# Performance work log

Hardware: AMD Instinct MI355X
Metric: run time of the kernel (lower is better)

## Reference

```python
import jax, jax.numpy as jnp
import numpy as np


def _conv(x, k):
    # x: (B,H,W,Cin), k: (kh,kw,Cin,Cout), SAME padding, stride 1
    return jax.lax.conv_general_dilated(
        x, k, window_strides=(1, 1), padding='SAME',
        dimension_numbers=('NHWC', 'HWIO', 'NHWC'))


def _hard_sigmoid(x):
    # Keras ConvLSTM2D default recurrent_activation='hard_sigmoid'
    return jnp.clip(0.2 * x + 0.5, 0.0, 1.0)


def _convlstm_layer(x_seq, k, rk, b):
    # x_seq: (B,T,H,W,Cin); gates packed i,f,c,o along channel axis (Keras order)
    B, T, H, W, _ = x_seq.shape
    F = rk.shape[2]
    h0 = jnp.zeros((B, H, W, F), x_seq.dtype)
    c0 = jnp.zeros((B, H, W, F), x_seq.dtype)

    def step(carry, xt):
        h, c = carry
        z = _conv(xt, k) + _conv(h, rk) + b
        i, f, g, o = jnp.split(z, 4, axis=-1)
        c_new = _hard_sigmoid(f) * c + _hard_sigmoid(i) * jnp.tanh(g)
        h_new = _hard_sigmoid(o) * jnp.tanh(c_new)
        return (h_new, c_new), h_new

    (h, c), ys = jax.lax.scan(step, (h0, c0), jnp.moveaxis(x_seq, 1, 0))
    return jnp.moveaxis(ys, 0, 1), h, c  # outputs (B,T,H,W,F), final h, c


def setup_inputs() -> dict:
    key = jax.random.key(0)
    ks = jax.random.split(key, 6)
    s = 0.05
    return {
        'x': jax.random.normal(ks[0], (8, 10, 64, 64, 1), jnp.float32),
        'k0': jax.random.normal(ks[1], (3, 3, 1, 256), jnp.float32) * s,
        'rk0': jax.random.normal(ks[2], (3, 3, 64, 256), jnp.float32) * s,
        'b0': jnp.zeros((256,), jnp.float32),
        'k1': jax.random.normal(ks[3], (3, 3, 64, 256), jnp.float32) * s,
        'rk1': jax.random.normal(ks[4], (3, 3, 64, 256), jnp.float32) * s,
        'b1': jnp.zeros((256,), jnp.float32),
    }


def reference(x, k0, rk0, b0, k1, rk1, b1):
    # layer 0
    seq0, h0, c0 = _convlstm_layer(x, k0, rk0, b0)
    # layer 1 consumes layer-0 sequence
    _, h1, c1 = _convlstm_layer(seq0, k1, rk1, b1)
    # states list [[h0,c0],[h1,c1]] -> stacked (layers=2, 2, B, H, W, F)
    return jnp.stack([jnp.stack([h0, c0]), jnp.stack([h1, c1])])
```

## Files before the change

### kernel.cpp

```cpp
#include <hip/hip_runtime.h>
#include <hip/hip_bf16.h>

typedef unsigned short u16;
typedef __attribute__((ext_vector_type(8))) short short8;
typedef __attribute__((ext_vector_type(4))) float f32x4;

#define T_STEPS 10
#define NB 8
#define HH 64
#define WW 64
#define FF 64
#define NGATE 256
#define HP 66
#define PIX (NB*HH*WW)
#define ROWCH 528

__device__ __forceinline__ u16 f2bf(float f) {
    unsigned u = __float_as_uint(f);
    u += 0x7FFF + ((u >> 16) & 1);
    return (u16)(u >> 16);
}
__device__ __forceinline__ float hsig(float x) {
    return fminf(fmaxf(0.2f * x + 0.5f, 0.0f), 1.0f);
}
__device__ __forceinline__ float ftanh(float x) {
    float e = __expf(2.0f * x);
    return 1.0f - 2.0f / (e + 1.0f);
}
__device__ __forceinline__ void gll16(const void* g, void* l) {
    __builtin_amdgcn_global_load_lds(
        (const __attribute__((address_space(1))) unsigned*)g,
        (__attribute__((address_space(3))) unsigned*)l, 16, 0, 0);
}

__global__ void wtrans_kernel(const float* __restrict__ W0,
                              const float* __restrict__ W1,
                              u16* __restrict__ BS, int K) {
    int total = (K >> 6) << 14;
    for (int o = blockIdx.x * blockDim.x + threadIdx.x; o < total;
         o += gridDim.x * blockDim.x) {
        int e = o & 7, lane = (o >> 3) & 63, g = (o >> 9) & 3;
        int ks = (o >> 11) & 1, fq = (o >> 12) & 3, kc = o >> 14;
        int quad = lane >> 4, l15 = lane & 15;
        int n = g * 64 + fq * 16 + l15;
        int k = kc * 64 + ks * 32 + quad * 8 + e;
        float v = (k < 576) ? W0[k * NGATE + n] : W1[(k - 576) * NGATE + n];
        BS[o] = f2bf(v);
    }
}

__global__ __launch_bounds__(256, 3)
void fused_step_kernel(const u16* __restrict__ h0_prev, u16* __restrict__ h0_new,
                       const u16* __restrict__ h1_prev, u16* __restrict__ h1_new,
                       const u16* __restrict__ B0S, const u16* __restrict__ B1S,
                       const float* __restrict__ x, const float* __restrict__ k0w,
                       const float* __restrict__ b0, const float* __restrict__ b1,
                       float* __restrict__ c0, float* __restrict__ c1,
                       float* __restrict__ oh0, float* __restrict__ oc0,
                       float* __restrict__ oh1, float* __restrict__ oc1,
                       int u) {
    int blk = blockIdx.x;
    int b = blk & 7;
    int k = blk >> 3;
    int c = k & 31, s = k >> 5;
    int role = (c + s) & 1;
    int y = c + ((s >> 1) << 5);
    int pxb = b * 64 + y;
    if (role == 0 && u >= T_STEPS) return;
    if (role == 1 && u == 0) return;

    __shared__ __align__(16) u16 sRows[3328 * 8];
    __shared__ float xs[3][WW + 2];

    int tid = threadIdx.x;
    int lane = tid & 63, fq = tid >> 6;
    int quad = lane >> 4, l15 = lane & 15;

    const u16* BS = role ? B1S : B0S;
    int nrows = role ? 6 : 3;
    int nstage = nrows * ROWCH;

    if (role == 0 && tid < 3 * (WW + 2)) {
        int dyi = tid / (WW + 2), xx = tid - dyi * (WW + 2);
        int yy = y + dyi - 1, col = xx - 1;
        float v = 0.0f;
        if (yy >= 0 && yy < HH && col >= 0 && col < WW)
            v = x[(((size_t)b * T_STEPS + u) * HH + yy) * WW + col];
        xs[dyi][xx] = v;
    }

    for (int j = 0; j < 13; ++j) {
        int q = tid + j * 256;
        if (q < nstage) {
            int r = q / ROWCH, rem = q - r * ROWCH;
            int px = rem >> 3, cb = (rem & 7) ^ (px & 7);
            const u16* src = (r < 3) ? h0_prev : h1_prev;
            int grow = y + ((r < 3) ? r : r - 3);
            gll16(src + ((size_t)(b * HP + grow) * HP + px) * FF + cb * 8,
                  &sRows[(size_t)q * 8]);
        }
    }
    asm volatile("s_waitcnt vmcnt(0) lgkmcnt(0)\n\ts_barrier" ::: "memory");

    f32x4 acc[4][4];
#pragma unroll
    for (int mt = 0; mt < 4; ++mt)
#pragma unroll
        for (int g = 0; g < 4; ++g)
            acc[mt][g] = (f32x4){0.f, 0.f, 0.f, 0.f};

#define TAP(KC, ROWBASE, DX)                                                  \
    {                                                                         \
        const u16* bp = BS + ((size_t)(KC) << 14) + (fq << 12) + lane * 8;    \
        short8 bF[8];                                                         \
        _Pragma("unroll")                                                     \
        for (int j = 0; j < 8; ++j)                                           \
            bF[j] = *(const short8*)(bp + ((size_t)j << 9));                  \
        _Pragma("unroll")                                                     \
        for (int ks = 0; ks < 2; ++ks) {                                      \
            short8 aF[4];                                                     \
            _Pragma("unroll")                                                 \
            for (int mt = 0; mt < 4; ++mt) {                                  \
                int px = mt * 16 + l15 + (DX) + 1;                            \
                int chunk = (ROWBASE) + px * 8 + ((ks * 4 + quad) ^ (px & 7));\
                aF[mt] = *(const short8*)&sRows[(size_t)chunk * 8];           \
            }                                                                 \
            _Pragma("unroll")                                                 \
            for (int mt = 0; mt < 4; ++mt)                                    \
                _Pragma("unroll")                                             \
                for (int g = 0; g < 4; ++g)                                   \
                    acc[mt][g] = __builtin_amdgcn_mfma_f32_16x16x32_bf16(     \
                        aF[mt], bF[ks * 4 + g], acc[mt][g], 0, 0, 0);         \
        }                                                                     \
    }

    if (role == 0) {
#pragma unroll
        for (int kc = 0; kc < 9; ++kc)
            TAP(kc, (kc / 3) * ROWCH, kc % 3 - 1);
    } else {
#pragma unroll
        for (int kc = 0; kc < 18; ++kc) {
            int t = (kc < 9) ? kc : kc - 9;
            int row = ((kc < 9) ? 0 : 3) + t / 3;
            TAP(kc, row * ROWCH, t % 3 - 1);
        }
    }

    const float* bias = role ? b1 : b0;
    float* cbuf = role ? c1 : c0;
    u16* hout = role ? h1_new : h0_new;
    int wo = role ? (u == T_STEPS) : (u == T_STEPS - 1);
    float* outh = role ? oh1 : oh0;
    float* outc = role ? oc1 : oc0;

    int f = fq * 16 + l15;
    float bi = bias[f], bff = bias[64 + f], bg = bias[128 + f], bo = bias[192 + f];
    float wk[4][9];
    if (role == 0) {
#pragma unroll
        for (int g = 0; g < 4; ++g)
#pragma unroll
            for (int tau = 0; tau < 9; ++tau)
                wk[g][tau] = k0w[tau * NGATE + g * 64 + f];
    }
#pragma unroll
    for (int mt = 0; mt < 4; ++mt) {
#pragma unroll
        for (int r = 0; r < 4; ++r) {
            int xcol = mt * 16 + quad * 4 + r;
            size_t p = (size_t)pxb * 64 + xcol;
            float zi = acc[mt][0][r] + bi;
            float zf = acc[mt][1][r] + bff;
            float zg = acc[mt][2][r] + bg;
            float zo = acc[mt][3][r] + bo;
            if (role == 0) {
#pragma unroll
                for (int tau = 0; tau < 9; ++tau) {
                    float xv = xs[tau / 3][xcol + tau % 3];
                    zi += xv * wk[0][tau];
                    zf += xv * wk[1][tau];
                    zg += xv * wk[2][tau];
                    zo += xv * wk[3][tau];
                }
            }
            float cold = cbuf[p * FF + f];
            float cn = hsig(zf) * cold + hsig(zi) * ftanh(zg);
            float hn = hsig(zo) * ftanh(cn);
            cbuf[p * FF + f] = cn;
            hout[(((size_t)(b * HP + y + 1)) * HP + (xcol + 1)) * FF + f] = f2bf(hn);
            if (wo) { outh[p * FF + f] = hn; outc[p * FF + f] = cn; }
        }
    }
}

extern "C" void kernel_launch(void* const* d_in, const int* in_sizes, int n_in,
                              void* d_out, int out_size, void* d_ws, size_t ws_size,
                              hipStream_t stream) {
    const float* x   = (const float*)d_in[0];
    const float* k0  = (const float*)d_in[1];
    const float* rk0 = (const float*)d_in[2];
    const float* b0  = (const float*)d_in[3];
    const float* k1  = (const float*)d_in[4];
    const float* rk1 = (const float*)d_in[5];
    const float* b1  = (const float*)d_in[6];
    float* out = (float*)d_out;

    char* ws = (char*)d_ws;
    const size_t HPAD_BYTES = (size_t)NB * HP * HP * FF * 2;
    const size_t C_BYTES    = (size_t)PIX * FF * 4;

    u16* h0p[2]; u16* h1p[2];
    h0p[0] = (u16*)(ws);
    h0p[1] = (u16*)(ws + HPAD_BYTES);
    h1p[0] = (u16*)(ws + 2 * HPAD_BYTES);
    h1p[1] = (u16*)(ws + 3 * HPAD_BYTES);
    float* c0 = (float*)(ws + 4 * HPAD_BYTES);
    float* c1 = (float*)(ws + 4 * HPAD_BYTES + C_BYTES);
    u16* B0S  = (u16*)(ws + 4 * HPAD_BYTES + 2 * C_BYTES);
    u16* B1S  = (u16*)(ws + 4 * HPAD_BYTES + 2 * C_BYTES + (size_t)9 * 16384 * 2);

    hipMemsetAsync(ws, 0, 4 * HPAD_BYTES + 2 * C_BYTES, stream);

    wtrans_kernel<<<512, 256, 0, stream>>>(rk0, rk0, B0S, 576);
    wtrans_kernel<<<512, 256, 0, stream>>>(k1, rk1, B1S, 1152);

    float* oh0 = out;
    float* oc0 = out + (size_t)PIX * FF;
    float* oh1 = out + 2 * (size_t)PIX * FF;
    float* oc1 = out + 3 * (size_t)PIX * FF;

    for (int u = 0; u <= T_STEPS; ++u) {
        const u16* h0_prev = h0p[(u + 1) & 1];
        u16*       h0_new  = h0p[u & 1];
        const u16* h1_prev = h1p[u & 1];
        u16*       h1_new  = h1p[(u + 1) & 1];
        fused_step_kernel<<<1024, 256, 0, stream>>>(
            h0_prev, h0_new, h1_prev, h1_new, B0S, B1S,
            x, k0, b0, b1, c0, c1, oh0, oc0, oh1, oc1, u);
    }
}
```

Measured before the change: 517.2 us.

## Split each row block across two filter halves and stage h rows in two phases

Each block now covers half of the 64 filters for one image row, so the grid doubles to 2048 blocks. The four waves split into a 2x2 arrangement over pixel halves and filter halves, which halves the accumulator registers. The layer-1 role stages the h0 rows and the h1 rows one after the other through a single 3-row LDS buffer instead of holding all six rows at once, and launch bounds rise to 4 blocks per CU. This cuts LDS and register use to raise occupancy and parallelism. The cost is that each h row is loaded twice (once per filter half) and the layer-1 path gets an extra barrier between its two phases.

```diff
diff --git a/kernel.cpp b/kernel.cpp
--- a/kernel.cpp
+++ b/kernel.cpp
@@ -14,6 +14,7 @@
 #define HP 66
 #define PIX (NB*HH*WW)
 #define ROWCH 528
+#define STAGECH (3*ROWCH)
 
 __device__ __forceinline__ u16 f2bf(float f) {
     unsigned u = __float_as_uint(f);
@@ -31,6 +32,12 @@
     __builtin_amdgcn_global_load_lds(
         (const __attribute__((address_space(1))) unsigned*)g,
         (__attribute__((address_space(3))) unsigned*)l, 16, 0, 0);
+}
+__device__ __forceinline__ void lds_barrier() {
+    asm volatile("s_waitcnt lgkmcnt(0)\n\ts_barrier" ::: "memory");
+}
+__device__ __forceinline__ void full_barrier() {
+    asm volatile("s_waitcnt vmcnt(0) lgkmcnt(0)\n\ts_barrier" ::: "memory");
 }
 
 __global__ void wtrans_kernel(const float* __restrict__ W0,
@@ -49,7 +56,7 @@
     }
 }
 
-__global__ __launch_bounds__(256, 3)
+__global__ __launch_bounds__(256, 4)
 void fused_step_kernel(const u16* __restrict__ h0_prev, u16* __restrict__ h0_new,
                        const u16* __restrict__ h1_prev, u16* __restrict__ h1_new,
                        const u16* __restrict__ B0S, const u16* __restrict__ B1S,
@@ -64,21 +71,21 @@
     int k = blk >> 3;
     int c = k & 31, s = k >> 5;
     int role = (c + s) & 1;
-    int y = c + ((s >> 1) << 5);
+    int idx = c + ((s >> 1) << 5);
+    int y = idx >> 1;
+    int nh = idx & 1;
     int pxb = b * 64 + y;
     if (role == 0 && u >= T_STEPS) return;
     if (role == 1 && u == 0) return;
 
-    __shared__ __align__(16) u16 sRows[3328 * 8];
+    __shared__ __align__(16) u16 sRows[STAGECH * 8];
     __shared__ float xs[3][WW + 2];
 
     int tid = threadIdx.x;
-    int lane = tid & 63, fq = tid >> 6;
+    int lane = tid & 63, wv = tid >> 6;
     int quad = lane >> 4, l15 = lane & 15;
-
-    const u16* BS = role ? B1S : B0S;
-    int nrows = role ? 6 : 3;
-    int nstage = nrows * ROWCH;
+    int mh = wv >> 1, fh = wv & 1;
+    int fqs = nh * 2 + fh;
 
     if (role == 0 && tid < 3 * (WW + 2)) {
         int dyi = tid / (WW + 2), xx = tid - dyi * (WW + 2);
@@ -89,44 +96,47 @@
         xs[dyi][xx] = v;
     }
 
-    for (int j = 0; j < 13; ++j) {
-        int q = tid + j * 256;
-        if (q < nstage) {
-            int r = q / ROWCH, rem = q - r * ROWCH;
-            int px = rem >> 3, cb = (rem & 7) ^ (px & 7);
-            const u16* src = (r < 3) ? h0_prev : h1_prev;
-            int grow = y + ((r < 3) ? r : r - 3);
-            gll16(src + ((size_t)(b * HP + grow) * HP + px) * FF + cb * 8,
-                  &sRows[(size_t)q * 8]);
-        }
-    }
-    asm volatile("s_waitcnt vmcnt(0) lgkmcnt(0)\n\ts_barrier" ::: "memory");
-
-    f32x4 acc[4][4];
-#pragma unroll
-    for (int mt = 0; mt < 4; ++mt)
+#define STAGE3(SRC)                                                           \
+    for (int j = 0; j < 7; ++j) {                                             \
+        int q = tid + j * 256;                                                \
+        if (q < STAGECH) {                                                    \
+            int r = q / ROWCH, rem = q - r * ROWCH;                           \
+            int px = rem >> 3, cb = (rem & 7) ^ (px & 7);                     \
+            gll16((SRC) + ((size_t)(b * HP + y + r) * HP + px) * FF + cb * 8, \
+                  &sRows[(size_t)q * 8]);                                     \
+        }                                                                     \
+    }
+
+    f32x4 acc[2][4];
+#pragma unroll
+    for (int mt = 0; mt < 2; ++mt)
 #pragma unroll
         for (int g = 0; g < 4; ++g)
             acc[mt][g] = (f32x4){0.f, 0.f, 0.f, 0.f};
 
-#define TAP(KC, ROWBASE, DX)                                                  \
-    {                                                                         \
-        const u16* bp = BS + ((size_t)(KC) << 14) + (fq << 12) + lane * 8;    \
+    const u16* BS = role ? B1S : B0S;
+
+#define TAPS9(KC0)                                                            \
+    _Pragma("unroll")                                                         \
+    for (int t = 0; t < 9; ++t) {                                             \
+        int rowbase = (t / 3) * ROWCH, dx = t % 3 - 1;                        \
+        const u16* bp = BS + ((size_t)((KC0) + t) << 14) + (fqs << 12)        \
+                      + lane * 8;                                             \
         short8 bF[8];                                                         \
         _Pragma("unroll")                                                     \
         for (int j = 0; j < 8; ++j)                                           \
             bF[j] = *(const short8*)(bp + ((size_t)j << 9));                  \
         _Pragma("unroll")                                                     \
         for (int ks = 0; ks < 2; ++ks) {                                      \
-            short8 aF[4];                                                     \
+            short8 aF[2];                                                     \
             _Pragma("unroll")                                                 \
-            for (int mt = 0; mt < 4; ++mt) {                                  \
-                int px = mt * 16 + l15 + (DX) + 1;                            \
-                int chunk = (ROWBASE) + px * 8 + ((ks * 4 + quad) ^ (px & 7));\
+            for (int mt = 0; mt < 2; ++mt) {                                  \
+                int px = mh * 32 + mt * 16 + l15 + dx + 1;                    \
+                int chunk = rowbase + px * 8 + ((ks * 4 + quad) ^ (px & 7));  \
                 aF[mt] = *(const short8*)&sRows[(size_t)chunk * 8];           \
             }                                                                 \
             _Pragma("unroll")                                                 \
-            for (int mt = 0; mt < 4; ++mt)                                    \
+            for (int mt = 0; mt < 2; ++mt)                                    \
                 _Pragma("unroll")                                             \
                 for (int g = 0; g < 4; ++g)                                   \
                     acc[mt][g] = __builtin_amdgcn_mfma_f32_16x16x32_bf16(     \
@@ -134,17 +144,14 @@
         }                                                                     \
     }
 
-    if (role == 0) {
-#pragma unroll
-        for (int kc = 0; kc < 9; ++kc)
-            TAP(kc, (kc / 3) * ROWCH, kc % 3 - 1);
-    } else {
-#pragma unroll
-        for (int kc = 0; kc < 18; ++kc) {
-            int t = (kc < 9) ? kc : kc - 9;
-            int row = ((kc < 9) ? 0 : 3) + t / 3;
-            TAP(kc, row * ROWCH, t % 3 - 1);
-        }
+    STAGE3(h0_prev);
+    full_barrier();
+    TAPS9(0);
+    if (role) {
+        lds_barrier();
+        STAGE3(h1_prev);
+        full_barrier();
+        TAPS9(9);
     }
 
     const float* bias = role ? b1 : b0;
@@ -154,7 +161,7 @@
     float* outh = role ? oh1 : oh0;
     float* outc = role ? oc1 : oc0;
 
-    int f = fq * 16 + l15;
+    int f = fqs * 16 + l15;
     float bi = bias[f], bff = bias[64 + f], bg = bias[128 + f], bo = bias[192 + f];
     float wk[4][9];
     if (role == 0) {
@@ -165,10 +172,10 @@
                 wk[g][tau] = k0w[tau * NGATE + g * 64 + f];
     }
 #pragma unroll
-    for (int mt = 0; mt < 4; ++mt) {
+    for (int mt = 0; mt < 2; ++mt) {
 #pragma unroll
         for (int r = 0; r < 4; ++r) {
-            int xcol = mt * 16 + quad * 4 + r;
+            int xcol = mh * 32 + mt * 16 + quad * 4 + r;
             size_t p = (size_t)pxb * 64 + xcol;
             float zi = acc[mt][0][r] + bi;
             float zf = acc[mt][1][r] + bff;
@@ -235,7 +242,7 @@
         u16*       h0_new  = h0p[u & 1];
         const u16* h1_prev = h1p[u & 1];
         u16*       h1_new  = h1p[(u + 1) & 1];
-        fused_step_kernel<<<1024, 256, 0, stream>>>(
+        fused_step_kernel<<<2048, 256, 0, stream>>>(
             h0_prev, h0_new, h1_prev, h1_new, B0S, B1S,
             x, k0, b0, b1, c0, c1, oh0, oc0, oh1, oc1, u);
     }
```

Result: slower. 540.1 us (+4.4%).
